# Performance work log

Hardware: AMD Instinct MI355X
Metric: run time of the kernel (lower is better)

## Reference

```python
import jax, jax.numpy as jnp
import numpy as np

EPS = 1e-5

def rms_norm(x, scale, eps=EPS):
    rms = jax.lax.rsqrt(jnp.mean(x * x, axis=-1, keepdims=True) + eps)
    return scale * (x * rms)

def act_quant(x, min_scale=0.001, max_scale=1000.0):
    # int8 activation quantization (STE in torch; fwd math only here)
    max_val = jnp.max(jnp.abs(x), axis=-1, keepdims=True)
    s = jnp.clip(127.0 / (max_val + 1e-5), min_scale, max_scale)
    return jnp.clip(jnp.round(s * x), -128.0, 127.0) / s

def weight_quant(w, num_bits=8):
    qmax = 2.0 ** (num_bits - 1) - 1.0
    scale = qmax / (jnp.max(jnp.abs(w)) + 1e-5)
    return jnp.round(jnp.clip(w * scale, -(qmax + 1.0), qmax)) / scale

def ternarize(w):
    sf = jnp.clip(1.0 / (jnp.mean(jnp.abs(w)) + 1e-5), 1e-4, 1e4)
    return jnp.sign(w * sf)

def setup_inputs() -> dict:
    key = jax.random.key(0)
    ks = jax.random.split(key, 5)
    B, S, E, H = 8, 512, 2048, 2048
    x = jax.random.normal(ks[0], (B, S, E), dtype=jnp.float32)
    # ternary {-1,0,1} init as in ternary_initialize
    def tern_init(k, shape):
        r = jax.random.uniform(k, shape, dtype=jnp.float32)
        return jnp.where(r < 1.0 / 3.0, -1.0, jnp.where(r > 2.0 / 3.0, 1.0, 0.0))
    return {
        "x": x,
        "rms_scale": jnp.ones((H,), jnp.float32),
        "W_f": tern_init(ks[1], (E, H)),
        "W_c": tern_init(ks[2], (E, H)),
        "W_g": tern_init(ks[3], (H, E)),
        "b_f": jnp.ones((H,), jnp.float32),
        "b_c": jnp.zeros((H,), jnp.float32),
        "b_g": jnp.zeros((H,), jnp.float32),
    }

def reference(x, rms_scale, W_f, W_c, W_g, b_f, b_c, b_g):
    B, S, E = x.shape
    H = W_f.shape[1]
    # quantize + ternarize weights once (identical every timestep)
    Wt_f = ternarize(weight_quant(W_f))
    Wt_c = ternarize(weight_quant(W_c))
    Wt_g = ternarize(weight_quant(W_g))  # (H, E) but E == H

    def step(h, x_t):
        xq = act_quant(rms_norm(x_t, rms_scale))
        # matmul-free linear: x @ (pos_mask - neg_mask) == x @ sign(W)
        f_t = jax.nn.sigmoid(xq @ Wt_f + b_f)
        c_t = jax.nn.silu(xq @ Wt_c + b_c)
        g_t = jax.nn.sigmoid(xq @ Wt_g + b_g)
        h_new = f_t * h + (1.0 - f_t) * c_t
        o_t = g_t * h_new
        # layer-level copy gate: sigmoid(W_g @ x_t^T)^T = sigmoid(x_t @ W_g^T), raw weights
        cg = jax.nn.sigmoid(x_t @ W_g.T)
        h_out = cg * x_t + (1.0 - cg) * h_new
        return h_out, o_t

    h0 = jnp.zeros((B, H), x.dtype)
    _, outs = jax.lax.scan(step, h0, jnp.swapaxes(x, 0, 1))  # scan over S
    return jnp.swapaxes(outs, 0, 1)  # (B, S, H)
```

## Files before the change

kernel.cpp:

```cpp
#include <hip/hip_runtime.h>
#include <hip/hip_bf16.h>
#include <cstdint>
#include <cstddef>

#define RTOT 4096
#define DIM  2048
#define NCAT 6144
#define NCHUNK 16
#define TCHUNK 32

typedef __attribute__((ext_vector_type(4))) int int4v;

__device__ __forceinline__ float fast_sigmoid(float z) {
    return __builtin_amdgcn_rcpf(1.0f + __expf(-z));
}
__device__ __forceinline__ unsigned short f2h(float f) {
    union { _Float16 h; unsigned short u; } v; v.h = (_Float16)f; return v.u;
}
__device__ __forceinline__ float h2f(unsigned short u) {
    union { _Float16 h; unsigned short u; } v; v.u = u; return (float)v.h;
}

#define GLDS(gp, lp) __builtin_amdgcn_global_load_lds( \
    (__attribute__((address_space(1))) const void*)(gp), \
    (__attribute__((address_space(3))) void*)(lp), 16, 0, 0)

__device__ __forceinline__ int4v frag_ld(const signed char* lds, int R, int lq) {
    return *(const int4v*)(lds + R * 64 + ((lq ^ ((R >> 1) & 3)) * 16));
}

__global__ __launch_bounds__(256) void prep_all(
    const float* __restrict__ x, const float* __restrict__ scale,
    const float* __restrict__ Wf, const float* __restrict__ Wc,
    const float* __restrict__ Wg,
    signed char* __restrict__ WcatT, signed char* __restrict__ Wgb,
    signed char* __restrict__ Xq, signed char* __restrict__ Q1,
    signed char* __restrict__ Q2, float* __restrict__ s_arr,
    float* __restrict__ s1_arr)
{
    __shared__ __align__(16) char smem[4224];
    int bid = blockIdx.x;
    int tid = threadIdx.x;
    if (bid < 3072) {
        signed char (*tile)[65] = (signed char(*)[65])smem;
        int j0 = (bid % 96) * 64;
        int k0 = (bid / 96) * 64;
        const float* W = (j0 < 2048) ? Wf : (j0 < 4096) ? Wc : Wg;
        int jb = j0 & 2047;
        int c  = tid & 63;
        int rr = tid >> 6;
#pragma unroll
        for (int p = 0; p < 16; ++p) {
            int kl = p * 4 + rr;
            tile[kl][c] = (signed char)(int)W[(size_t)(k0 + kl) * DIM + jb + c];
        }
        __syncthreads();
#pragma unroll
        for (int p = 0; p < 16; ++p) {
            int jl = p * 4 + rr;
            WcatT[(size_t)(j0 + jl) * DIM + k0 + c] = tile[c][jl];
        }
    } else if (bid < 4096) {
        int idx = (bid - 3072) * 4096 + tid * 16;
#pragma unroll
        for (int p = 0; p < 4; ++p) {
            float4 v = *(const float4*)(Wg + idx + p * 4);
            char4 o;
            o.x = (signed char)(int)v.x; o.y = (signed char)(int)v.y;
            o.z = (signed char)(int)v.z; o.w = (signed char)(int)v.w;
            *(char4*)(Wgb + idx + p * 4) = o;
        }
    } else {
        float* red = (float*)smem;
        float* tot = (float*)(smem + 64);
        int row = bid - 4096;
        const float* xr = x + (size_t)row * DIM + tid * 8;
        const float* sr = scale + tid * 8;
        float4 a0 = *(const float4*)(xr);
        float4 a1 = *(const float4*)(xr + 4);
        float4 c0 = *(const float4*)(sr);
        float4 c1 = *(const float4*)(sr + 4);
        float xs[8] = {a0.x, a0.y, a0.z, a0.w, a1.x, a1.y, a1.z, a1.w};
        float sc[8] = {c0.x, c0.y, c0.z, c0.w, c1.x, c1.y, c1.z, c1.w};
        float sum = 0.f, mx2 = 0.f;
#pragma unroll
        for (int i = 0; i < 8; ++i) {
            sum += xs[i] * xs[i];
            mx2 = fmaxf(mx2, fabsf(xs[i]));
        }
#pragma unroll
        for (int off = 32; off > 0; off >>= 1) {
            sum += __shfl_down(sum, off);
            mx2 = fmaxf(mx2, __shfl_down(mx2, off));
        }
        int lane = tid & 63, wv = tid >> 6;
        if (lane == 0) { red[wv] = sum; red[4 + wv] = mx2; }
        __syncthreads();
        if (tid == 0) {
            tot[0] = red[0] + red[1] + red[2] + red[3];
            tot[1] = fmaxf(fmaxf(red[4], red[5]), fmaxf(red[6], red[7]));
        }
        __syncthreads();
        float rms = 1.0f / sqrtf(tot[0] * (1.0f / 2048.0f) + 1e-5f);
        float y[8]; float mx = 0.f;
#pragma unroll
        for (int i = 0; i < 8; ++i) {
            y[i] = (xs[i] * rms) * sc[i];
            mx = fmaxf(mx, fabsf(y[i]));
        }
#pragma unroll
        for (int off = 32; off > 0; off >>= 1) mx = fmaxf(mx, __shfl_down(mx, off));
        if (lane == 0) red[8 + wv] = mx;
        __syncthreads();
        if (tid == 0)
            tot[2] = fmaxf(fmaxf(red[8], red[9]), fmaxf(red[10], red[11]));
        __syncthreads();
        float s = 127.0f / (tot[2] + 1e-5f);
        s = fminf(fmaxf(s, 0.001f), 1000.0f);
        float s1 = 127.0f / (tot[1] + 1e-5f);
        float inv_s1 = 1.0f / s1;
        if (tid == 0) { s_arr[row] = s; s1_arr[row] = s1; }
        signed char q8[8], q1b[8], q2b[8];
#pragma unroll
        for (int i = 0; i < 8; ++i) {
            float q = fminf(fmaxf(rintf(s * y[i]), -128.f), 127.f);
            q8[i] = (signed char)(int)q;
            float qq1 = fminf(fmaxf(rintf(s1 * xs[i]), -128.f), 127.f);
            q1b[i] = (signed char)(int)qq1;
            float r = xs[i] - qq1 * inv_s1;
            float qq2 = fminf(fmaxf(rintf(s1 * 256.f * r), -128.f), 127.f);
            q2b[i] = (signed char)(int)qq2;
        }
        size_t o = (size_t)row * DIM + tid * 8;
        *(int2*)(Xq + o) = *(int2*)q8;
        *(int2*)(Q1 + o) = *(int2*)q1b;
        *(int2*)(Q2 + o) = *(int2*)q2b;
    }
}

__global__ __launch_bounds__(256) void gemm_all(
    const signed char* __restrict__ Xq, const signed char* __restrict__ WcatT,
    const signed char* __restrict__ Q1, const signed char* __restrict__ Q2,
    const signed char* __restrict__ Wgb,
    const float* __restrict__ s_arr, const float* __restrict__ s1_arr,
    const float* __restrict__ b_f, const float* __restrict__ b_c,
    const float* __restrict__ b_g,
    unsigned short* __restrict__ FCG,
    unsigned short* __restrict__ U,
    unsigned short* __restrict__ V)
{
    __shared__ __align__(16) signed char lds[32768];
    int bid = blockIdx.x;
    int grp = bid / 5, r5 = bid % 5;
    int tid = threadIdx.x;
    int lane = tid & 63, wv = tid >> 6;
    int lr = lane & 15, lq = lane >> 4;
    int rA = lane >> 2;
    int gch = ((lane & 3) ^ ((lane >> 3) & 3)) * 16;

    if (r5 < 3) {
        int fb = grp * 3 + r5;
        int m0 = (fb / 48) * 128;
        int n0 = (fb % 48) * 128;
        int wm = (wv >> 1) * 64, wn = (wv & 1) * 64;
        const signed char* Ab = Xq + (size_t)m0 * DIM;
        const signed char* Bb = WcatT + (size_t)n0 * DIM;

        int4v acc[4][4] = {};
#pragma unroll
        for (int it = 0; it < 2; ++it) {
            int region = wv + it * 4;
            int rr = region * 16 + rA;
            GLDS(Ab + (size_t)rr * DIM + gch, lds + region * 1024);
            GLDS(Bb + (size_t)rr * DIM + gch, lds + 8192 + region * 1024);
        }
        for (int k6 = 0; k6 < 32; ++k6) {
            signed char* cur = lds + (k6 & 1) * 16384;
            signed char* nxt = lds + ((k6 + 1) & 1) * 16384;
            __syncthreads();
            if (k6 + 1 < 32) {
                int kt = (k6 + 1) * 64;
#pragma unroll
                for (int it = 0; it < 2; ++it) {
                    int region = wv + it * 4;
                    int rr = region * 16 + rA;
                    GLDS(Ab + (size_t)rr * DIM + kt + gch, nxt + region * 1024);
                    GLDS(Bb + (size_t)rr * DIM + kt + gch, nxt + 8192 + region * 1024);
                }
            }
            int4v af[4], bb[4];
#pragma unroll
            for (int i = 0; i < 4; ++i) af[i] = frag_ld(cur, wm + i * 16 + lr, lq);
#pragma unroll
            for (int j = 0; j < 4; ++j) bb[j] = frag_ld(cur + 8192, wn + j * 16 + lr, lq);
#pragma unroll
            for (int i = 0; i < 4; ++i)
#pragma unroll
                for (int j = 0; j < 4; ++j)
                    acc[i][j] = __builtin_amdgcn_mfma_i32_16x16x64_i8(
                        af[i], bb[j], acc[i][j], 0, 0, 0);
        }
#pragma unroll
        for (int i = 0; i < 4; ++i) {
            float rinv[4];
#pragma unroll
            for (int r = 0; r < 4; ++r)
                rinv[r] = __builtin_amdgcn_rcpf(s_arr[m0 + wm + i * 16 + lq * 4 + r]);
#pragma unroll
            for (int j = 0; j < 4; ++j) {
                int gcol = n0 + wn + j * 16 + lr;
                int sec = gcol >> 11;
                int jj = gcol & 2047;
                float bias = (sec == 0) ? b_f[jj] : (sec == 1) ? b_c[jj] : b_g[jj];
#pragma unroll
                for (int r = 0; r < 4; ++r) {
                    int grow = m0 + wm + i * 16 + lq * 4 + r;
                    float z = fmaf((float)acc[i][j][r], rinv[r], bias);
                    float sg = fast_sigmoid(z);
                    FCG[(size_t)grow * NCAT + gcol] = f2h((sec == 1) ? z * sg : sg);
                }
            }
        }
    } else {
        int cb = grp * 2 + (r5 - 3);
        int m0 = (cb >> 4) * 64;
        int n0 = (cb & 15) * 128;
        int wm = (wv >> 1) * 32, wn = (wv & 1) * 64;
        const signed char* A1b = Q1 + (size_t)m0 * DIM;
        const signed char* A2b = Q2 + (size_t)m0 * DIM;
        const signed char* Bb  = Wgb + (size_t)n0 * DIM;
        int r1 = wv * 16 + rA;

        int4v acc1[2][4] = {};
        int4v acc2[2][4] = {};
        {
            GLDS(A1b + (size_t)r1 * DIM + gch, lds + wv * 1024);
            GLDS(A2b + (size_t)r1 * DIM + gch, lds + 4096 + wv * 1024);
#pragma unroll
            for (int it = 0; it < 2; ++it) {
                int region = wv + it * 4;
                int rr = region * 16 + rA;
                GLDS(Bb + (size_t)rr * DIM + gch, lds + 8192 + region * 1024);
            }
        }
        for (int k6 = 0; k6 < 32; ++k6) {
            signed char* cur = lds + (k6 & 1) * 16384;
            signed char* nxt = lds + ((k6 + 1) & 1) * 16384;
            __syncthreads();
            if (k6 + 1 < 32) {
                int kt = (k6 + 1) * 64;
                GLDS(A1b + (size_t)r1 * DIM + kt + gch, nxt + wv * 1024);
                GLDS(A2b + (size_t)r1 * DIM + kt + gch, nxt + 4096 + wv * 1024);
#pragma unroll
                for (int it = 0; it < 2; ++it) {
                    int region = wv + it * 4;
                    int rr = region * 16 + rA;
                    GLDS(Bb + (size_t)rr * DIM + kt + gch, nxt + 8192 + region * 1024);
                }
            }
            int4v bb[4];
#pragma unroll
            for (int j = 0; j < 4; ++j) bb[j] = frag_ld(cur + 8192, wn + j * 16 + lr, lq);
#pragma unroll
            for (int i = 0; i < 2; ++i) {
                int4v a1 = frag_ld(cur, wm + i * 16 + lr, lq);
                int4v a2 = frag_ld(cur + 4096, wm + i * 16 + lr, lq);
#pragma unroll
                for (int j = 0; j < 4; ++j) {
                    acc1[i][j] = __builtin_amdgcn_mfma_i32_16x16x64_i8(
                        a1, bb[j], acc1[i][j], 0, 0, 0);
                    acc2[i][j] = __builtin_amdgcn_mfma_i32_16x16x64_i8(
                        a2, bb[j], acc2[i][j], 0, 0, 0);
                }
            }
        }
#pragma unroll
        for (int i = 0; i < 2; ++i) {
            float rinv[4];
#pragma unroll
            for (int r = 0; r < 4; ++r)
                rinv[r] = __builtin_amdgcn_rcpf(s1_arr[m0 + wm + i * 16 + lq * 4 + r]);
#pragma unroll
            for (int j = 0; j < 4; ++j) {
                int gcol = n0 + wn + j * 16 + lr;
#pragma unroll
                for (int r = 0; r < 4; ++r) {
                    int grow = m0 + wm + i * 16 + lq * 4 + r;
                    size_t go = (size_t)grow * DIM + gcol;
                    float zs = (float)acc1[i][j][r] + (float)acc2[i][j][r] * (1.f / 256.f);
                    float cg = fast_sigmoid(zs * rinv[r]);
                    float xv = ((float)Q1[go] + (float)Q2[go] * (1.f / 256.f)) * rinv[r];
                    U[go] = f2h(cg * xv);
                    V[go] = f2h(1.f - cg);
                }
            }
        }
    }
}

__global__ __launch_bounds__(256) void scan_partial(
    const unsigned short* __restrict__ FCG, const unsigned short* __restrict__ U,
    const unsigned short* __restrict__ V, float4* __restrict__ PQ4)
{
    int tp = blockIdx.x * 256 + threadIdx.x;
    int c = blockIdx.y;
    int b = blockIdx.z;
    int h0 = tp * 2;
    size_t r0 = (size_t)(b * 512 + c * TCHUNK);
    const unsigned short* fp = FCG + r0 * NCAT + h0;
    const unsigned short* up = U + r0 * DIM + h0;
    const unsigned short* vp = V + r0 * DIM + h0;
    float P0 = 1.f, Q0 = 0.f, P1 = 1.f, Q1v = 0.f;
#pragma unroll 4
    for (int t = 0; t < TCHUNK; ++t) {
        unsigned fw = *(const unsigned*)(fp);
        unsigned cw = *(const unsigned*)(fp + 2048);
        unsigned uw = *(const unsigned*)(up);
        unsigned vw = *(const unsigned*)(vp);
        float f0 = h2f(fw & 0xffff), f1 = h2f(fw >> 16);
        float c0 = h2f(cw & 0xffff), c1 = h2f(cw >> 16);
        float u0 = h2f(uw & 0xffff), u1 = h2f(uw >> 16);
        float v0 = h2f(vw & 0xffff), v1 = h2f(vw >> 16);
        float A0 = v0 * f0, A1 = v1 * f1;
        float B0 = fmaf(v0 * (1.f - f0), c0, u0);
        float B1 = fmaf(v1 * (1.f - f1), c1, u1);
        P0 = A0 * P0; Q0 = fmaf(A0, Q0, B0);
        P1 = A1 * P1; Q1v = fmaf(A1, Q1v, B1);
        fp += NCAT; up += DIM; vp += DIM;
    }
    float4 o; o.x = P0; o.y = Q0; o.z = P1; o.w = Q1v;
    PQ4[(size_t)c * 8192 + b * 1024 + tp] = o;
}

__global__ __launch_bounds__(256) void scan_final(
    const unsigned short* __restrict__ FCG, const unsigned short* __restrict__ U,
    const unsigned short* __restrict__ V, const float4* __restrict__ PQ4,
    float* __restrict__ out)
{
    int tp = blockIdx.x * 256 + threadIdx.x;
    int c = blockIdx.y;
    int b = blockIdx.z;
    int h0 = tp * 2;
    float h0s = 0.f, h1s = 0.f;
    for (int cc = 0; cc < c; ++cc) {
        float4 pq = PQ4[(size_t)cc * 8192 + b * 1024 + tp];
        h0s = fmaf(pq.x, h0s, pq.y);
        h1s = fmaf(pq.z, h1s, pq.w);
    }
    size_t r0 = (size_t)(b * 512 + c * TCHUNK);
    const unsigned short* fp = FCG + r0 * NCAT + h0;
    const unsigned short* up = U + r0 * DIM + h0;
    const unsigned short* vp = V + r0 * DIM + h0;
    float* op = out + r0 * DIM + h0;
#pragma unroll 4
    for (int t = 0; t < TCHUNK; ++t) {
        unsigned fw = *(const unsigned*)(fp);
        unsigned cw = *(const unsigned*)(fp + 2048);
        unsigned gw = *(const unsigned*)(fp + 4096);
        unsigned uw = *(const unsigned*)(up);
        unsigned vw = *(const unsigned*)(vp);
        float f0 = h2f(fw & 0xffff), f1 = h2f(fw >> 16);
        float c0 = h2f(cw & 0xffff), c1 = h2f(cw >> 16);
        float g0 = h2f(gw & 0xffff), g1 = h2f(gw >> 16);
        float u0 = h2f(uw & 0xffff), u1 = h2f(uw >> 16);
        float v0 = h2f(vw & 0xffff), v1 = h2f(vw >> 16);
        float hn0 = f0 * h0s + (1.f - f0) * c0;
        float hn1 = f1 * h1s + (1.f - f1) * c1;
        float2 ov; ov.x = g0 * hn0; ov.y = g1 * hn1;
        *(float2*)op = ov;
        h0s = fmaf(v0, hn0, u0);
        h1s = fmaf(v1, hn1, u1);
        fp += NCAT; up += DIM; vp += DIM; op += DIM;
    }
}

extern "C" void kernel_launch(void* const* d_in, const int* in_sizes, int n_in,
                              void* d_out, int out_size, void* d_ws, size_t ws_size,
                              hipStream_t stream) {
    const float* x     = (const float*)d_in[0];
    const float* rmssc = (const float*)d_in[1];
    const float* W_f   = (const float*)d_in[2];
    const float* W_c   = (const float*)d_in[3];
    const float* W_g   = (const float*)d_in[4];
    const float* b_f   = (const float*)d_in[5];
    const float* b_c   = (const float*)d_in[6];
    const float* b_g   = (const float*)d_in[7];
    float* out = (float*)d_out;

    char* ws = (char*)d_ws;
    size_t off = 0;
    auto alloc = [&](size_t bytes) -> void* {
        void* p = ws + off;
        off += (bytes + 255) & ~(size_t)255;
        return p;
    };
    signed char* WcatT = (signed char*)alloc((size_t)NCAT * DIM);
    signed char* Wgb   = (signed char*)alloc((size_t)DIM * DIM);
    signed char* Xq    = (signed char*)alloc((size_t)RTOT * DIM);
    signed char* Q1    = (signed char*)alloc((size_t)RTOT * DIM);
    signed char* Q2    = (signed char*)alloc((size_t)RTOT * DIM);
    float* s_arr       = (float*)alloc((size_t)RTOT * 4);
    float* s1_arr      = (float*)alloc((size_t)RTOT * 4);
    unsigned short* FCG = (unsigned short*)alloc((size_t)RTOT * NCAT * 2);
    unsigned short* U   = (unsigned short*)alloc((size_t)RTOT * DIM * 2);
    unsigned short* V   = (unsigned short*)alloc((size_t)RTOT * DIM * 2);
    float4* PQ4        = (float4*)alloc((size_t)NCHUNK * 8192 * 16);

    hipLaunchKernelGGL(prep_all, dim3(8192), dim3(256), 0, stream,
                       x, rmssc, W_f, W_c, W_g, WcatT, Wgb, Xq, Q1, Q2,
                       s_arr, s1_arr);
    hipLaunchKernelGGL(gemm_all, dim3(2560), dim3(256), 0, stream,
                       Xq, WcatT, Q1, Q2, Wgb, s_arr, s1_arr,
                       b_f, b_c, b_g, FCG, U, V);
    hipLaunchKernelGGL(scan_partial, dim3(DIM / 512, NCHUNK, 8), dim3(256), 0, stream,
                       FCG, U, V, PQ4);
    hipLaunchKernelGGL(scan_final, dim3(DIM / 512, NCHUNK, 8), dim3(256), 0, stream,
                       FCG, U, V, PQ4, out);
}
```

Baseline: 298.1 us.

## Restructure int8 GEMM into 256x256 tiles with triple-buffered ping-pong pipeline

Rewrites the fused int8 MFMA GEMM kernel to use 512-thread blocks with 256x256 (and 256x128 for the copy-gate) output tiles. A three-stage LDS ring buffer is filled via direct global-to-LDS loads, and the loads are interleaved with four MFMA phases per k-step using explicit barriers, waitcnts and setprio. The aim is better data reuse per tile and hiding memory latency behind matrix work. In exchange it needs 120KB of dynamic LDS, which allows one block per CU despite launch_bounds(512,2), and many block-wide barriers per iteration.

```diff
diff --git a/kernel.cpp b/kernel.cpp
--- a/kernel.cpp
+++ b/kernel.cpp
@@ -8,6 +8,7 @@
 #define NCAT 6144
 #define NCHUNK 16
 #define TCHUNK 32
+#define NT 32
 
 typedef __attribute__((ext_vector_type(4))) int int4v;
 
@@ -25,8 +26,8 @@
     (__attribute__((address_space(1))) const void*)(gp), \
     (__attribute__((address_space(3))) void*)(lp), 16, 0, 0)
 
-__device__ __forceinline__ int4v frag_ld(const signed char* lds, int R, int lq) {
-    return *(const int4v*)(lds + R * 64 + ((lq ^ ((R >> 1) & 3)) * 16));
+__device__ __forceinline__ int4v frag_ld(const signed char* p, int R, int lq) {
+    return *(const int4v*)(p + R * 64 + ((lq ^ ((R >> 1) & 3)) * 16));
 }
 
 __global__ __launch_bounds__(256) void prep_all(
@@ -93,8 +94,8 @@
             sum += __shfl_down(sum, off);
             mx2 = fmaxf(mx2, __shfl_down(mx2, off));
         }
-        int lane = tid & 63, wv = tid >> 6;
-        if (lane == 0) { red[wv] = sum; red[4 + wv] = mx2; }
+        int lane = tid & 63, wvv = tid >> 6;
+        if (lane == 0) { red[wvv] = sum; red[4 + wvv] = mx2; }
         __syncthreads();
         if (tid == 0) {
             tot[0] = red[0] + red[1] + red[2] + red[3];
@@ -110,7 +111,7 @@
         }
 #pragma unroll
         for (int off = 32; off > 0; off >>= 1) mx = fmaxf(mx, __shfl_down(mx, off));
-        if (lane == 0) red[8 + wv] = mx;
+        if (lane == 0) red[8 + wvv] = mx;
         __syncthreads();
         if (tid == 0)
             tot[2] = fmaxf(fmaxf(red[8], red[9]), fmaxf(red[10], red[11]));
@@ -138,7 +139,7 @@
     }
 }
 
-__global__ __launch_bounds__(256) void gemm_all(
+__global__ __launch_bounds__(512, 2) void gemm_all(
     const signed char* __restrict__ Xq, const signed char* __restrict__ WcatT,
     const signed char* __restrict__ Q1, const signed char* __restrict__ Q2,
     const signed char* __restrict__ Wgb,
@@ -149,73 +150,137 @@
     unsigned short* __restrict__ U,
     unsigned short* __restrict__ V)
 {
-    __shared__ __align__(16) signed char lds[32768];
+    extern __shared__ __align__(16) signed char lds[];
     int bid = blockIdx.x;
     int grp = bid / 5, r5 = bid % 5;
     int tid = threadIdx.x;
     int lane = tid & 63, wv = tid >> 6;
     int lr = lane & 15, lq = lane >> 4;
-    int rA = lane >> 2;
-    int gch = ((lane & 3) ^ ((lane >> 3) & 3)) * 16;
+    int srow = wv * 16 + (lane >> 2);
+    int ssw  = ((lane & 3) ^ ((srow >> 1) & 3)) * 16;
+    const size_t ustep = (size_t)128 * DIM;
 
     if (r5 < 3) {
         int fb = grp * 3 + r5;
-        int m0 = (fb / 48) * 128;
-        int n0 = (fb % 48) * 128;
-        int wm = (wv >> 1) * 64, wn = (wv & 1) * 64;
+        int m0 = (fb & 15) * 256;
+        int n0 = (fb >> 4) * 256;
+        int wm = (wv >> 2) * 128;
+        int wn = (wv & 3) * 64;
         const signed char* Ab = Xq + (size_t)m0 * DIM;
         const signed char* Bb = WcatT + (size_t)n0 * DIM;
-
-        int4v acc[4][4] = {};
-#pragma unroll
-        for (int it = 0; it < 2; ++it) {
-            int region = wv + it * 4;
-            int rr = region * 16 + rA;
-            GLDS(Ab + (size_t)rr * DIM + gch, lds + region * 1024);
-            GLDS(Bb + (size_t)rr * DIM + gch, lds + 8192 + region * 1024);
-        }
-        for (int k6 = 0; k6 < 32; ++k6) {
-            signed char* cur = lds + (k6 & 1) * 16384;
-            signed char* nxt = lds + ((k6 + 1) & 1) * 16384;
-            __syncthreads();
-            if (k6 + 1 < 32) {
-                int kt = (k6 + 1) * 64;
-#pragma unroll
-                for (int it = 0; it < 2; ++it) {
-                    int region = wv + it * 4;
-                    int rr = region * 16 + rA;
-                    GLDS(Ab + (size_t)rr * DIM + kt + gch, nxt + region * 1024);
-                    GLDS(Bb + (size_t)rr * DIM + kt + gch, nxt + 8192 + region * 1024);
-                }
-            }
-            int4v af[4], bb[4];
-#pragma unroll
-            for (int i = 0; i < 4; ++i) af[i] = frag_ld(cur, wm + i * 16 + lr, lq);
-#pragma unroll
-            for (int j = 0; j < 4; ++j) bb[j] = frag_ld(cur + 8192, wn + j * 16 + lr, lq);
-#pragma unroll
-            for (int i = 0; i < 4; ++i)
-#pragma unroll
-                for (int j = 0; j < 4; ++j)
+        const signed char* gA = Ab + (size_t)srow * DIM + ssw;
+        const signed char* gB = Bb + (size_t)srow * DIM + ssw;
+
+        int4v acc[8][4] = {};
+        int4v a[4], b[4];
+
+#pragma unroll
+        for (int t0 = 0; t0 < 2; ++t0) {
+            signed char* sb = lds + t0 * 32768;
+            GLDS(gA + t0 * 64,         sb + wv * 1024);
+            GLDS(gA + ustep + t0 * 64, sb + 8192 + wv * 1024);
+            GLDS(gB + t0 * 64,         sb + 16384 + wv * 1024);
+            GLDS(gB + ustep + t0 * 64, sb + 16384 + 8192 + wv * 1024);
+        }
+
+        int bc = 0, bn = 1, bs = 2;
+        for (int t = 0; t < NT; ++t) {
+            if (t == NT - 1) { asm volatile("s_waitcnt vmcnt(0)" ::: "memory"); }
+            else             { asm volatile("s_waitcnt vmcnt(4)" ::: "memory"); }
+            __builtin_amdgcn_sched_barrier(0);
+            __builtin_amdgcn_s_barrier();
+            __builtin_amdgcn_sched_barrier(0);
+            const signed char* cA = lds + bc * 32768;
+            const signed char* cB = cA + 16384;
+            signed char* sA = lds + bs * 32768;
+            signed char* sB = sA + 16384;
+            int kt2 = (t + 2) * 64;
+            bool st = (t + 2 < NT);
+
+#pragma unroll
+            for (int i = 0; i < 4; ++i) a[i] = frag_ld(cA, wm + i * 16 + lr, lq);
+#pragma unroll
+            for (int j = 0; j < 2; ++j) b[j] = frag_ld(cB, wn + j * 16 + lr, lq);
+            if (st) GLDS(gA + kt2, sA + wv * 1024);
+            __builtin_amdgcn_s_barrier();
+            asm volatile("s_waitcnt lgkmcnt(0)" ::: "memory");
+            __builtin_amdgcn_sched_barrier(0);
+            __builtin_amdgcn_s_setprio(1);
+#pragma unroll
+            for (int i = 0; i < 4; ++i)
+#pragma unroll
+                for (int j = 0; j < 2; ++j)
                     acc[i][j] = __builtin_amdgcn_mfma_i32_16x16x64_i8(
-                        af[i], bb[j], acc[i][j], 0, 0, 0);
-        }
-#pragma unroll
-        for (int i = 0; i < 4; ++i) {
+                        a[i], b[j], acc[i][j], 0, 0, 0);
+            __builtin_amdgcn_s_setprio(0);
+            __builtin_amdgcn_s_barrier();
+
+#pragma unroll
+            for (int j = 2; j < 4; ++j) b[j] = frag_ld(cB, wn + j * 16 + lr, lq);
+            if (st) GLDS(gA + ustep + kt2, sA + 8192 + wv * 1024);
+            __builtin_amdgcn_s_barrier();
+            asm volatile("s_waitcnt lgkmcnt(0)" ::: "memory");
+            __builtin_amdgcn_sched_barrier(0);
+            __builtin_amdgcn_s_setprio(1);
+#pragma unroll
+            for (int i = 0; i < 4; ++i)
+#pragma unroll
+                for (int j = 2; j < 4; ++j)
+                    acc[i][j] = __builtin_amdgcn_mfma_i32_16x16x64_i8(
+                        a[i], b[j], acc[i][j], 0, 0, 0);
+            __builtin_amdgcn_s_setprio(0);
+            __builtin_amdgcn_s_barrier();
+
+#pragma unroll
+            for (int i = 0; i < 4; ++i) a[i] = frag_ld(cA, wm + (4 + i) * 16 + lr, lq);
+            if (st) GLDS(gB + kt2, sB + wv * 1024);
+            __builtin_amdgcn_s_barrier();
+            asm volatile("s_waitcnt lgkmcnt(0)" ::: "memory");
+            __builtin_amdgcn_sched_barrier(0);
+            __builtin_amdgcn_s_setprio(1);
+#pragma unroll
+            for (int i = 0; i < 4; ++i)
+#pragma unroll
+                for (int j = 0; j < 2; ++j)
+                    acc[4 + i][j] = __builtin_amdgcn_mfma_i32_16x16x64_i8(
+                        a[i], b[j], acc[4 + i][j], 0, 0, 0);
+            __builtin_amdgcn_s_setprio(0);
+            __builtin_amdgcn_s_barrier();
+
+            if (st) GLDS(gB + ustep + kt2, sB + 8192 + wv * 1024);
+            __builtin_amdgcn_s_barrier();
+            asm volatile("s_waitcnt lgkmcnt(0)" ::: "memory");
+            __builtin_amdgcn_sched_barrier(0);
+            __builtin_amdgcn_s_setprio(1);
+#pragma unroll
+            for (int i = 0; i < 4; ++i)
+#pragma unroll
+                for (int j = 2; j < 4; ++j)
+                    acc[4 + i][j] = __builtin_amdgcn_mfma_i32_16x16x64_i8(
+                        a[i], b[j], acc[4 + i][j], 0, 0, 0);
+            __builtin_amdgcn_s_setprio(0);
+            __builtin_amdgcn_s_barrier();
+
+            int tmp = bc; bc = bn; bn = bs; bs = tmp;
+        }
+
+        int rowb = m0 + wm;
+#pragma unroll
+        for (int mi = 0; mi < 8; ++mi) {
             float rinv[4];
 #pragma unroll
             for (int r = 0; r < 4; ++r)
-                rinv[r] = __builtin_amdgcn_rcpf(s_arr[m0 + wm + i * 16 + lq * 4 + r]);
-#pragma unroll
-            for (int j = 0; j < 4; ++j) {
-                int gcol = n0 + wn + j * 16 + lr;
+                rinv[r] = __builtin_amdgcn_rcpf(s_arr[rowb + mi * 16 + lq * 4 + r]);
+#pragma unroll
+            for (int ni = 0; ni < 4; ++ni) {
+                int gcol = n0 + wn + ni * 16 + lr;
                 int sec = gcol >> 11;
                 int jj = gcol & 2047;
                 float bias = (sec == 0) ? b_f[jj] : (sec == 1) ? b_c[jj] : b_g[jj];
 #pragma unroll
                 for (int r = 0; r < 4; ++r) {
-                    int grow = m0 + wm + i * 16 + lq * 4 + r;
-                    float z = fmaf((float)acc[i][j][r], rinv[r], bias);
+                    int grow = rowb + mi * 16 + lq * 4 + r;
+                    float z = fmaf((float)acc[mi][ni][r], rinv[r], bias);
                     float sg = fast_sigmoid(z);
                     FCG[(size_t)grow * NCAT + gcol] = f2h((sec == 1) ? z * sg : sg);
                 }
@@ -223,71 +288,134 @@
         }
     } else {
         int cb = grp * 2 + (r5 - 3);
-        int m0 = (cb >> 4) * 64;
-        int n0 = (cb & 15) * 128;
-        int wm = (wv >> 1) * 32, wn = (wv & 1) * 64;
+        int m0 = (cb & 15) * 256;
+        int n0 = (cb >> 4) * 128;
+        int wm = (wv >> 2) * 128;
+        int wn = (wv & 3) * 32;
         const signed char* A1b = Q1 + (size_t)m0 * DIM;
         const signed char* A2b = Q2 + (size_t)m0 * DIM;
         const signed char* Bb  = Wgb + (size_t)n0 * DIM;
-        int r1 = wv * 16 + rA;
-
-        int4v acc1[2][4] = {};
-        int4v acc2[2][4] = {};
-        {
-            GLDS(A1b + (size_t)r1 * DIM + gch, lds + wv * 1024);
-            GLDS(A2b + (size_t)r1 * DIM + gch, lds + 4096 + wv * 1024);
-#pragma unroll
-            for (int it = 0; it < 2; ++it) {
-                int region = wv + it * 4;
-                int rr = region * 16 + rA;
-                GLDS(Bb + (size_t)rr * DIM + gch, lds + 8192 + region * 1024);
+        const signed char* g1 = A1b + (size_t)srow * DIM + ssw;
+        const signed char* g2 = A2b + (size_t)srow * DIM + ssw;
+        const signed char* gB = Bb + (size_t)srow * DIM + ssw;
+
+        int4v acc1[8][2] = {};
+        int4v acc2[8][2] = {};
+        int4v a1[4], a2[4], b[2];
+
+#pragma unroll
+        for (int t0 = 0; t0 < 2; ++t0) {
+            signed char* sb = lds + t0 * 40960;
+            GLDS(g1 + t0 * 64,         sb + wv * 1024);
+            GLDS(g1 + ustep + t0 * 64, sb + 8192 + wv * 1024);
+            GLDS(gB + t0 * 64,         sb + 32768 + wv * 1024);
+            GLDS(g2 + t0 * 64,         sb + 16384 + wv * 1024);
+            GLDS(g2 + ustep + t0 * 64, sb + 16384 + 8192 + wv * 1024);
+        }
+
+        int bc = 0, bn = 1, bs = 2;
+        for (int t = 0; t < NT; ++t) {
+            if (t == NT - 1) { asm volatile("s_waitcnt vmcnt(0)" ::: "memory"); }
+            else             { asm volatile("s_waitcnt vmcnt(5)" ::: "memory"); }
+            __builtin_amdgcn_sched_barrier(0);
+            __builtin_amdgcn_s_barrier();
+            __builtin_amdgcn_sched_barrier(0);
+            const signed char* cA1 = lds + bc * 40960;
+            const signed char* cA2 = cA1 + 16384;
+            const signed char* cB  = cA1 + 32768;
+            signed char* s1p = lds + bs * 40960;
+            signed char* s2p = s1p + 16384;
+            signed char* sBp = s1p + 32768;
+            int kt2 = (t + 2) * 64;
+            bool st = (t + 2 < NT);
+
+#pragma unroll
+            for (int i = 0; i < 4; ++i) a1[i] = frag_ld(cA1, wm + i * 16 + lr, lq);
+#pragma unroll
+            for (int j = 0; j < 2; ++j) b[j] = frag_ld(cB, wn + j * 16 + lr, lq);
+            if (st) GLDS(g1 + kt2, s1p + wv * 1024);
+            __builtin_amdgcn_s_barrier();
+            asm volatile("s_waitcnt lgkmcnt(0)" ::: "memory");
+            __builtin_amdgcn_sched_barrier(0);
+            __builtin_amdgcn_s_setprio(1);
+#pragma unroll
+            for (int i = 0; i < 4; ++i)
+#pragma unroll
+                for (int j = 0; j < 2; ++j)
+                    acc1[i][j] = __builtin_amdgcn_mfma_i32_16x16x64_i8(
+                        a1[i], b[j], acc1[i][j], 0, 0, 0);
+            __builtin_amdgcn_s_setprio(0);
+            __builtin_amdgcn_s_barrier();
+
+#pragma unroll
+            for (int i = 0; i < 4; ++i) a2[i] = frag_ld(cA2, wm + i * 16 + lr, lq);
+            if (st) {
+                GLDS(g1 + ustep + kt2, s1p + 8192 + wv * 1024);
+                GLDS(gB + kt2, sBp + wv * 1024);
             }
-        }
-        for (int k6 = 0; k6 < 32; ++k6) {
-            signed char* cur = lds + (k6 & 1) * 16384;
-            signed char* nxt = lds + ((k6 + 1) & 1) * 16384;
-            __syncthreads();
-            if (k6 + 1 < 32) {
-                int kt = (k6 + 1) * 64;
-                GLDS(A1b + (size_t)r1 * DIM + kt + gch, nxt + wv * 1024);
-                GLDS(A2b + (size_t)r1 * DIM + kt + gch, nxt + 4096 + wv * 1024);
-#pragma unroll
-                for (int it = 0; it < 2; ++it) {
-                    int region = wv + it * 4;
-                    int rr = region * 16 + rA;
-                    GLDS(Bb + (size_t)rr * DIM + kt + gch, nxt + 8192 + region * 1024);
-                }
-            }
-            int4v bb[4];
-#pragma unroll
-            for (int j = 0; j < 4; ++j) bb[j] = frag_ld(cur + 8192, wn + j * 16 + lr, lq);
-#pragma unroll
-            for (int i = 0; i < 2; ++i) {
-                int4v a1 = frag_ld(cur, wm + i * 16 + lr, lq);
-                int4v a2 = frag_ld(cur + 4096, wm + i * 16 + lr, lq);
-#pragma unroll
-                for (int j = 0; j < 4; ++j) {
-                    acc1[i][j] = __builtin_amdgcn_mfma_i32_16x16x64_i8(
-                        a1, bb[j], acc1[i][j], 0, 0, 0);
+            __builtin_amdgcn_s_barrier();
+            asm volatile("s_waitcnt lgkmcnt(0)" ::: "memory");
+            __builtin_amdgcn_sched_barrier(0);
+            __builtin_amdgcn_s_setprio(1);
+#pragma unroll
+            for (int i = 0; i < 4; ++i)
+#pragma unroll
+                for (int j = 0; j < 2; ++j)
                     acc2[i][j] = __builtin_amdgcn_mfma_i32_16x16x64_i8(
-                        a2, bb[j], acc2[i][j], 0, 0, 0);
-                }
-            }
-        }
-#pragma unroll
-        for (int i = 0; i < 2; ++i) {
+                        a2[i], b[j], acc2[i][j], 0, 0, 0);
+            __builtin_amdgcn_s_setprio(0);
+            __builtin_amdgcn_s_barrier();
+
+#pragma unroll
+            for (int i = 0; i < 4; ++i) a1[i] = frag_ld(cA1, wm + (4 + i) * 16 + lr, lq);
+            if (st) GLDS(g2 + kt2, s2p + wv * 1024);
+            __builtin_amdgcn_s_barrier();
+            asm volatile("s_waitcnt lgkmcnt(0)" ::: "memory");
+            __builtin_amdgcn_sched_barrier(0);
+            __builtin_amdgcn_s_setprio(1);
+#pragma unroll
+            for (int i = 0; i < 4; ++i)
+#pragma unroll
+                for (int j = 0; j < 2; ++j)
+                    acc1[4 + i][j] = __builtin_amdgcn_mfma_i32_16x16x64_i8(
+                        a1[i], b[j], acc1[4 + i][j], 0, 0, 0);
+            __builtin_amdgcn_s_setprio(0);
+            __builtin_amdgcn_s_barrier();
+
+#pragma unroll
+            for (int i = 0; i < 4; ++i) a2[i] = frag_ld(cA2, wm + (4 + i) * 16 + lr, lq);
+            if (st) GLDS(g2 + ustep + kt2, s2p + 8192 + wv * 1024);
+            __builtin_amdgcn_s_barrier();
+            asm volatile("s_waitcnt lgkmcnt(0)" ::: "memory");
+            __builtin_amdgcn_sched_barrier(0);
+            __builtin_amdgcn_s_setprio(1);
+#pragma unroll
+            for (int i = 0; i < 4; ++i)
+#pragma unroll
+                for (int j = 0; j < 2; ++j)
+                    acc2[4 + i][j] = __builtin_amdgcn_mfma_i32_16x16x64_i8(
+                        a2[i], b[j], acc2[4 + i][j], 0, 0, 0);
+            __builtin_amdgcn_s_setprio(0);
+            __builtin_amdgcn_s_barrier();
+
+            int tmp = bc; bc = bn; bn = bs; bs = tmp;
+        }
+
+        int rowb = m0 + wm;
+#pragma unroll
+        for (int mi = 0; mi < 8; ++mi) {
             float rinv[4];
 #pragma unroll
             for (int r = 0; r < 4; ++r)
-                rinv[r] = __builtin_amdgcn_rcpf(s1_arr[m0 + wm + i * 16 + lq * 4 + r]);
-#pragma unroll
-            for (int j = 0; j < 4; ++j) {
-                int gcol = n0 + wn + j * 16 + lr;
+                rinv[r] = __builtin_amdgcn_rcpf(s1_arr[rowb + mi * 16 + lq * 4 + r]);
+#pragma unroll
+            for (int ni = 0; ni < 2; ++ni) {
+                int gcol = n0 + wn + ni * 16 + lr;
 #pragma unroll
                 for (int r = 0; r < 4; ++r) {
-                    int grow = m0 + wm + i * 16 + lq * 4 + r;
+                    int grow = rowb + mi * 16 + lq * 4 + r;
                     size_t go = (size_t)grow * DIM + gcol;
-                    float zs = (float)acc1[i][j][r] + (float)acc2[i][j][r] * (1.f / 256.f);
+                    float zs = (float)acc1[mi][ni][r] + (float)acc2[mi][ni][r] * (1.f / 256.f);
                     float cg = fast_sigmoid(zs * rinv[r]);
                     float xv = ((float)Q1[go] + (float)Q2[go] * (1.f / 256.f)) * rinv[r];
                     U[go] = f2h(cg * xv);
@@ -406,10 +534,16 @@
     unsigned short* V   = (unsigned short*)alloc((size_t)RTOT * DIM * 2);
     float4* PQ4        = (float4*)alloc((size_t)NCHUNK * 8192 * 16);
 
+    static int gemm_attr_once = [](){
+        return (int)hipFuncSetAttribute((const void*)gemm_all,
+                   hipFuncAttributeMaxDynamicSharedMemorySize, 3 * 40960);
+    }();
+    (void)gemm_attr_once;
+
     hipLaunchKernelGGL(prep_all, dim3(8192), dim3(256), 0, stream,
                        x, rmssc, W_f, W_c, W_g, WcatT, Wgb, Xq, Q1, Q2,
                        s_arr, s1_arr);
-    hipLaunchKernelGGL(gemm_all, dim3(2560), dim3(256), 0, stream,
+    hipLaunchKernelGGL(gemm_all, dim3(640), dim3(512), 3 * 40960, stream,
                        Xq, WcatT, Q1, Q2, Wgb, s_arr, s1_arr,
                        b_f, b_c, b_g, FCG, U, V);
     hipLaunchKernelGGL(scan_partial, dim3(DIM / 512, NCHUNK, 8), dim3(256), 0, stream,
```

Result: faster. 277.6 us (-6.9%).
